# Performance work log

Measured on AMD Instinct MI355X. Metric: run time of the kernel, lower is better.

## Reference

```python
import jax, jax.numpy as jnp
import numpy as np

B = 4096      # batch of stimuli
U = 4096      # max_nunits
D = 16        # n_dims


def setup_inputs() -> dict:
    key = jax.random.key(0)
    k1, k2, k3 = jax.random.split(key, 3)
    # forward arg: stimuli, shaped [B, 1, D] so they broadcast against the U unit batch dim
    inp = jax.random.normal(k1, (B, 1, D), dtype=jnp.float32)
    # learned params (torch inits units to zeros; use small randn so outputs are nontrivial)
    units = 0.5 * jax.random.normal(k2, (U, D), dtype=jnp.float32)
    # attn param is [U, D, D]; module forces it diagonal each call. Build diagonal with
    # positive per-dim scales (torch init would be sqrt(0.02) * I per unit).
    diag = jax.random.uniform(k3, (U, D), dtype=jnp.float32, minval=0.05, maxval=0.3)
    attn = jax.vmap(jnp.diag)(diag)  # [U, D, D]
    return {"input": inp, "units": units, "attn": attn}


def reference(input, units, attn):
    # diag of scale_tril = per-dim std dev, clamped like torch.clamp(min=1e-6)
    diag = jnp.clip(jnp.diagonal(attn, axis1=-2, axis2=-1), 1e-6)  # [U, D]
    # MVN with scale_tril = diag(s): logpdf = -0.5*sum(((x-mu)/s)^2) - sum(log s) - 0.5*D*log(2pi)
    z = (input - units) / diag                       # [B, U, D] via broadcasting
    half_log_2pi = 0.5 * jnp.float32(np.log(2.0 * np.pi))
    log_prob = (-0.5 * jnp.sum(z * z, axis=-1)       # [B, U]
                - jnp.sum(jnp.log(diag), axis=-1)    # [U]
                - jnp.float32(D) * half_log_2pi)
    return jnp.exp(log_prob)                         # activations, [B, U]
```

## Files before the change

kernel.cpp:

```cpp
#include <hip/hip_runtime.h>
#include <hip/hip_bf16.h>
#include <math.h>


#define TPB 256
#define DD  16
#define UB  128
#define BB  128

typedef float v2f __attribute__((ext_vector_type(2)));

static constexpr float L2E   = 1.4426950408889634f;
static constexpr float HL2PI = 0.91893853320467274f;

__global__ __launch_bounds__(TPB, 4) void mva_tile(
    const float* __restrict__ x,
    const float* __restrict__ units,
    const float* __restrict__ attn,
    float* __restrict__ out,
    int U)
{
    const int tid = threadIdx.x;
    const int k   = blockIdx.x;
    const int xcd = k & 7;
    const int j   = k >> 3;
    const int uc  = xcd * 4 + (j & 3);
    const int bc  = j >> 2;
    const int u_base = uc * UB;
    const int b_base = bc * BB;

    __shared__ float xs[BB][DD];
    __shared__ float a1L[DD][UB + 2];
    __shared__ float a2L[DD][UB + 2];
    __shared__ float bp[2][UB];

    {
        const int ul   = tid & 127;
        const int half = tid >> 7;
        const int d0   = half * 8;
        const int u    = u_base + ul;
        const float* ar = attn + (size_t)u * DD * DD;
        float4 m0 = *reinterpret_cast<const float4*>(units + (size_t)u * DD + d0);
        float4 m1 = *reinterpret_cast<const float4*>(units + (size_t)u * DD + d0 + 4);
        const float mu[8] = {m0.x, m0.y, m0.z, m0.w, m1.x, m1.y, m1.z, m1.w};
        float bn = 0.f;
#pragma unroll
        for (int dd = 0; dd < 8; ++dd) {
            const int d = d0 + dd;
            float s = fmaxf(ar[d * (DD + 1)], 1e-6f);
            float w = 1.f / (s * s);
            a1L[d][ul] = L2E * mu[dd] * w;
            a2L[d][ul] = -0.5f * L2E * w;
            bn += -0.5f * mu[dd] * mu[dd] * w - logf(s);
        }
        bp[half][ul] = bn;
    }

    const float* xb = x + (size_t)b_base * DD;
#pragma unroll
    for (int r = 0; r < (BB * DD) / (TPB * 4); ++r) {
        const int q = (r * TPB + tid) * 4;
        *reinterpret_cast<float4*>(&xs[0][0] + q) =
            *reinterpret_cast<const float4*>(xb + q);
    }
    __syncthreads();

    const int up = tid & 63;
    const int br = tid >> 6;
    v2f a1p[DD], a2p[DD];
#pragma unroll
    for (int d = 0; d < DD; ++d) {
        a1p[d] = *reinterpret_cast<const v2f*>(&a1L[d][up * 2]);
        a2p[d] = *reinterpret_cast<const v2f*>(&a2L[d][up * 2]);
    }
    v2f biasp;
    {
        v2f b0 = *reinterpret_cast<const v2f*>(&bp[0][up * 2]);
        v2f b1 = *reinterpret_cast<const v2f*>(&bp[1][up * 2]);
        biasp[0] = L2E * (b0[0] + b1[0] - DD * HL2PI);
        biasp[1] = L2E * (b0[1] + b1[1] - DD * HL2PI);
    }

    float* orow = out + (size_t)b_base * U + u_base + up * 2;
#pragma unroll 2
    for (int it = 0; it < BB / 4; ++it) {
        const int b = it * 4 + br;
        v2f acc = biasp;
#pragma unroll
        for (int jj = 0; jj < 4; ++jj) {
            float4 xv = *reinterpret_cast<const float4*>(&xs[b][4 * jj]);
            const int d = 4 * jj;
            v2f xx, t;
            xx = (v2f){xv.x, xv.x};
            t   = __builtin_elementwise_fma(xx, a2p[d + 0], a1p[d + 0]);
            acc = __builtin_elementwise_fma(xx, t, acc);
            xx = (v2f){xv.y, xv.y};
            t   = __builtin_elementwise_fma(xx, a2p[d + 1], a1p[d + 1]);
            acc = __builtin_elementwise_fma(xx, t, acc);
            xx = (v2f){xv.z, xv.z};
            t   = __builtin_elementwise_fma(xx, a2p[d + 2], a1p[d + 2]);
            acc = __builtin_elementwise_fma(xx, t, acc);
            xx = (v2f){xv.w, xv.w};
            t   = __builtin_elementwise_fma(xx, a2p[d + 3], a1p[d + 3]);
            acc = __builtin_elementwise_fma(xx, t, acc);
        }
        float2 o;
        o.x = __builtin_amdgcn_exp2f(acc[0]);
        o.y = __builtin_amdgcn_exp2f(acc[1]);
        *reinterpret_cast<float2*>(orow + (size_t)b * U) = o;
    }
}

extern "C" void kernel_launch(void* const* d_in, const int* in_sizes, int n_in,
                              void* d_out, int out_size, void* d_ws, size_t ws_size,
                              hipStream_t stream) {
    const float* x     = (const float*)d_in[0];
    const float* units = (const float*)d_in[1];
    const float* attn  = (const float*)d_in[2];
    float* out = (float*)d_out;

    const int B = in_sizes[0] / DD;
    const int U = in_sizes[1] / DD;

    const int nblk = (U / UB) * (B / BB);
    mva_tile<<<nblk, TPB, 0, stream>>>(x, units, attn, out, U);
}
```

Measured before the change: 25.34 us.

## Stream stimuli via wave-uniform scalar loads instead of LDS staging; simplify bias math

The kernel no longer stages the stimulus tile in shared memory. Each wave now reads its stimulus rows directly with a wave-uniform index, so the loads can become scalar loads, and it prefetches the next row while computing the current one. The per-unit setup uses a hardware reciprocal and one log of the product of scales instead of eight logs. The inner loop switches from packed to scalar FMAs. The XCD-aware block remapping is replaced by a plain 2D grid, which may give up L2 locality across chiplets. These changes aim to cut LDS traffic, barrier cost and setup latency, at a small cost in precision.

```diff
diff --git a/kernel.cpp b/kernel.cpp
--- a/kernel.cpp
+++ b/kernel.cpp
@@ -5,34 +5,29 @@
 
 #define TPB 256
 #define DD  16
-#define UB  128
-#define BB  128
+#define UBL 128
+#define BBL 128
+#define NIT (BBL / 4)
 
 typedef float v2f __attribute__((ext_vector_type(2)));
 
 static constexpr float L2E   = 1.4426950408889634f;
 static constexpr float HL2PI = 0.91893853320467274f;
 
-__global__ __launch_bounds__(TPB, 4) void mva_tile(
+__global__ __launch_bounds__(TPB, 4) void mva_sx(
     const float* __restrict__ x,
     const float* __restrict__ units,
     const float* __restrict__ attn,
     float* __restrict__ out,
     int U)
 {
-    const int tid = threadIdx.x;
-    const int k   = blockIdx.x;
-    const int xcd = k & 7;
-    const int j   = k >> 3;
-    const int uc  = xcd * 4 + (j & 3);
-    const int bc  = j >> 2;
-    const int u_base = uc * UB;
-    const int b_base = bc * BB;
+    const int tid    = threadIdx.x;
+    const int u_base = blockIdx.x * UBL;
+    const int b_base = blockIdx.y * BBL;
 
-    __shared__ float xs[BB][DD];
-    __shared__ float a1L[DD][UB + 2];
-    __shared__ float a2L[DD][UB + 2];
-    __shared__ float bp[2][UB];
+    __shared__ float  a1L[DD][UBL + 2];
+    __shared__ float  a2L[DD][UBL + 2];
+    __shared__ float2 bpL[2][UBL];
 
     {
         const int ul   = tid & 127;
@@ -43,71 +38,70 @@
         float4 m0 = *reinterpret_cast<const float4*>(units + (size_t)u * DD + d0);
         float4 m1 = *reinterpret_cast<const float4*>(units + (size_t)u * DD + d0 + 4);
         const float mu[8] = {m0.x, m0.y, m0.z, m0.w, m1.x, m1.y, m1.z, m1.w};
-        float bn = 0.f;
+        float qn = 0.f, prod = 1.f;
 #pragma unroll
-        for (int dd = 0; dd < 8; ++dd) {
-            const int d = d0 + dd;
+        for (int k = 0; k < 8; ++k) {
+            const int d = d0 + k;
             float s = fmaxf(ar[d * (DD + 1)], 1e-6f);
-            float w = 1.f / (s * s);
-            a1L[d][ul] = L2E * mu[dd] * w;
+            float r = __builtin_amdgcn_rcpf(s);
+            float w = r * r;
+            a1L[d][ul] = L2E * mu[k] * w;
             a2L[d][ul] = -0.5f * L2E * w;
-            bn += -0.5f * mu[dd] * mu[dd] * w - logf(s);
+            qn   = fmaf(mu[k] * w, mu[k], qn);
+            prod *= s;
         }
-        bp[half][ul] = bn;
-    }
-
-    const float* xb = x + (size_t)b_base * DD;
-#pragma unroll
-    for (int r = 0; r < (BB * DD) / (TPB * 4); ++r) {
-        const int q = (r * TPB + tid) * 4;
-        *reinterpret_cast<float4*>(&xs[0][0] + q) =
-            *reinterpret_cast<const float4*>(xb + q);
+        bpL[half][ul] = make_float2(qn, __builtin_amdgcn_logf(prod));
     }
     __syncthreads();
 
     const int up = tid & 63;
-    const int br = tid >> 6;
+    const int wv = __builtin_amdgcn_readfirstlane(tid >> 6);
     v2f a1p[DD], a2p[DD];
 #pragma unroll
     for (int d = 0; d < DD; ++d) {
         a1p[d] = *reinterpret_cast<const v2f*>(&a1L[d][up * 2]);
         a2p[d] = *reinterpret_cast<const v2f*>(&a2L[d][up * 2]);
     }
-    v2f biasp;
+    float bias0, bias1;
     {
-        v2f b0 = *reinterpret_cast<const v2f*>(&bp[0][up * 2]);
-        v2f b1 = *reinterpret_cast<const v2f*>(&bp[1][up * 2]);
-        biasp[0] = L2E * (b0[0] + b1[0] - DD * HL2PI);
-        biasp[1] = L2E * (b0[1] + b1[1] - DD * HL2PI);
+        float2 qa = bpL[0][up * 2],     qb = bpL[1][up * 2];
+        float2 ra = bpL[0][up * 2 + 1], rb = bpL[1][up * 2 + 1];
+        bias0 = fmaf(-0.5f * L2E, qa.x + qb.x, -(qa.y + qb.y) - DD * L2E * HL2PI);
+        bias1 = fmaf(-0.5f * L2E, ra.x + rb.x, -(ra.y + rb.y) - DD * L2E * HL2PI);
     }
 
-    float* orow = out + (size_t)b_base * U + u_base + up * 2;
+    const float* xw = x + (size_t)(b_base + wv) * DD;
+    float* ow = out + (size_t)(b_base + wv) * U + u_base + up * 2;
+
+    float4 xa = *reinterpret_cast<const float4*>(xw + 0);
+    float4 xb = *reinterpret_cast<const float4*>(xw + 4);
+    float4 xc = *reinterpret_cast<const float4*>(xw + 8);
+    float4 xd = *reinterpret_cast<const float4*>(xw + 12);
+
 #pragma unroll 2
-    for (int it = 0; it < BB / 4; ++it) {
-        const int b = it * 4 + br;
-        v2f acc = biasp;
-#pragma unroll
-        for (int jj = 0; jj < 4; ++jj) {
-            float4 xv = *reinterpret_cast<const float4*>(&xs[b][4 * jj]);
-            const int d = 4 * jj;
-            v2f xx, t;
-            xx = (v2f){xv.x, xv.x};
-            t   = __builtin_elementwise_fma(xx, a2p[d + 0], a1p[d + 0]);
-            acc = __builtin_elementwise_fma(xx, t, acc);
-            xx = (v2f){xv.y, xv.y};
-            t   = __builtin_elementwise_fma(xx, a2p[d + 1], a1p[d + 1]);
-            acc = __builtin_elementwise_fma(xx, t, acc);
-            xx = (v2f){xv.z, xv.z};
-            t   = __builtin_elementwise_fma(xx, a2p[d + 2], a1p[d + 2]);
-            acc = __builtin_elementwise_fma(xx, t, acc);
-            xx = (v2f){xv.w, xv.w};
-            t   = __builtin_elementwise_fma(xx, a2p[d + 3], a1p[d + 3]);
-            acc = __builtin_elementwise_fma(xx, t, acc);
+    for (int it = 0; it < NIT; ++it) {
+        const float4 c0 = xa, c1 = xb, c2 = xc, c3 = xd;
+        if (it + 1 < NIT) {
+            const float* xn = xw + (size_t)(it + 1) * 4 * DD;
+            xa = *reinterpret_cast<const float4*>(xn + 0);
+            xb = *reinterpret_cast<const float4*>(xn + 4);
+            xc = *reinterpret_cast<const float4*>(xn + 8);
+            xd = *reinterpret_cast<const float4*>(xn + 12);
         }
+        float acc0 = bias0, acc1 = bias1;
+        float t;
+#define STEP(C, DK) \
+        t = fmaf(C, a2p[DK][0], a1p[DK][0]); acc0 = fmaf(C, t, acc0); \
+        t = fmaf(C, a2p[DK][1], a1p[DK][1]); acc1 = fmaf(C, t, acc1);
+        STEP(c0.x, 0)  STEP(c0.y, 1)  STEP(c0.z, 2)  STEP(c0.w, 3)
+        STEP(c1.x, 4)  STEP(c1.y, 5)  STEP(c1.z, 6)  STEP(c1.w, 7)
+        STEP(c2.x, 8)  STEP(c2.y, 9)  STEP(c2.z, 10) STEP(c2.w, 11)
+        STEP(c3.x, 12) STEP(c3.y, 13) STEP(c3.z, 14) STEP(c3.w, 15)
+#undef STEP
         float2 o;
-        o.x = __builtin_amdgcn_exp2f(acc[0]);
-        o.y = __builtin_amdgcn_exp2f(acc[1]);
-        *reinterpret_cast<float2*>(orow + (size_t)b * U) = o;
+        o.x = __builtin_amdgcn_exp2f(acc0);
+        o.y = __builtin_amdgcn_exp2f(acc1);
+        *reinterpret_cast<float2*>(ow + (size_t)it * 4 * U) = o;
     }
 }
 
@@ -122,6 +116,6 @@
     const int B = in_sizes[0] / DD;
     const int U = in_sizes[1] / DD;
 
-    const int nblk = (U / UB) * (B / BB);
-    mva_tile<<<nblk, TPB, 0, stream>>>(x, units, attn, out, U);
+    dim3 grid(U / UBL, B / BBL);
+    mva_sx<<<grid, TPB, 0, stream>>>(x, units, attn, out, U);
 }
```

Result: slower. 32.91 us (+29.9%).
